# Performance work log

Hardware: AMD Instinct MI355X
Metric: run time of the kernel (lower is better)

The kernel has to match this reference:

```python
import jax, jax.numpy as jnp
import numpy as np

# Channel pairs (disjoint), matching init_kwargs
PAIRS = np.array([[2 * i, 2 * i + 1] for i in range(16)], dtype=np.int32)  # [P, 2]


def setup_inputs() -> dict:
    key = jax.random.key(0)
    kx, km = jax.random.split(key)
    B, C, T = 128, 64, 8000
    X = jax.random.normal(kx, (B, C, T), dtype=jnp.float32)
    # p_symmetry = 0.5 Bernoulli swap mask, precomputed (original uses numpy rng)
    swap_mask = jax.random.bernoulli(km, 0.5, (B, PAIRS.shape[0]))  # [B, P] bool
    return {"X": X, "swap_mask": swap_mask}


def reference(X, swap_mask):
    # X: [B, C, T], swap_mask: [B, P] bool
    B, C, T = X.shape
    c1 = jnp.asarray(PAIRS[:, 0])  # [P]
    c2 = jnp.asarray(PAIRS[:, 1])  # [P]
    # Build a per-batch channel permutation: identity, except swapped pairs.
    perm = jnp.broadcast_to(jnp.arange(C, dtype=jnp.int32), (B, C))
    perm = perm.at[:, c1].set(jnp.where(swap_mask, c2[None, :], c1[None, :]))
    perm = perm.at[:, c2].set(jnp.where(swap_mask, c1[None, :], c2[None, :]))
    # Single fused gather over the channel axis: [B, C, T]
    return jnp.take_along_axis(X, perm[:, :, None], axis=1)
```

## Files before the change

### kernel.cpp

```cpp
#include <hip/hip_runtime.h>


#define B_DIM 128
#define C_DIM 64
#define T_DIM 8000
#define T4    (T_DIM / 4)
#define P_DIM 16

typedef float f4 __attribute__((ext_vector_type(4)));

__global__ __launch_bounds__(256) void
ChannelSymmetry_42339787603992_kernel(const f4* __restrict__ X,
                                      const unsigned char* __restrict__ mask,
                                      f4* __restrict__ Y) {
    const int row = blockIdx.x;
    const int b   = row >> 6;
    const int c   = row & 63;

    __shared__ int s_bytepacked;
    if (threadIdx.x == 0) s_bytepacked = 0;
    __syncthreads();
    {
        const unsigned int w = ((const unsigned int*)mask)[threadIdx.x];
        const bool hit = (w & 0xFFFFFF00u) != 0;
        if (__any(hit) && (threadIdx.x & 63) == 0) atomicOr(&s_bytepacked, 1);
    }
    __syncthreads();

    int sc = c;
    if (c < 32) {
        const int ms = s_bytepacked ? 1 : 4;
        const unsigned char sw = mask[(b * P_DIM + (c >> 1)) * ms];
        if (sw) sc = c ^ 1;
    }

    const f4* __restrict__ src = X + (size_t)((b << 6) | sc) * T4;
    f4* __restrict__       dst = Y + (size_t)row * T4;
    for (int col = threadIdx.x; col < T4; col += 256) {
        const f4 v = __builtin_nontemporal_load(&src[col]);
        __builtin_nontemporal_store(v, &dst[col]);
    }
}

extern "C" void kernel_launch(void* const* d_in, const int* in_sizes, int n_in,
                              void* d_out, int out_size, void* d_ws, size_t ws_size,
                              hipStream_t stream) {
    const f4*            X    = (const f4*)d_in[0];
    const unsigned char* mask = (const unsigned char*)d_in[1];
    f4*                  Y    = (f4*)d_out;

    const int grid = B_DIM * C_DIM;
    ChannelSymmetry_42339787603992_kernel<<<grid, 256, 0, stream>>>(X, mask, Y);
}
```

Before: 98.30 us.

## Flatten gather to one float4 per thread across a global grid

Replaces the one-block-per-row loop with a flat grid in which each thread copies a single float4, working out row and column by division. The mask-layout detection now uses a wavefront vote instead of shared memory with atomics and two barriers, and the nontemporal load/store builtins are dropped in favour of plain accesses. The aim is to remove per-block barrier overhead and the tail imbalance of 2000 float4 spread over 256 threads, in exchange for many more blocks, a per-thread integer divide, and a redundant mask read in every thread.

```diff
diff --git a/kernel.cpp b/kernel.cpp
--- a/kernel.cpp
+++ b/kernel.cpp
@@ -6,6 +6,7 @@
 #define T_DIM 8000
 #define T4    (T_DIM / 4)
 #define P_DIM 16
+#define N_F4  (B_DIM * C_DIM * T4)
 
 typedef float f4 __attribute__((ext_vector_type(4)));
 
@@ -13,33 +14,23 @@
 ChannelSymmetry_42339787603992_kernel(const f4* __restrict__ X,
                                       const unsigned char* __restrict__ mask,
                                       f4* __restrict__ Y) {
-    const int row = blockIdx.x;
-    const int b   = row >> 6;
-    const int c   = row & 63;
+    const unsigned g = blockIdx.x * 256u + threadIdx.x;
 
-    __shared__ int s_bytepacked;
-    if (threadIdx.x == 0) s_bytepacked = 0;
-    __syncthreads();
-    {
-        const unsigned int w = ((const unsigned int*)mask)[threadIdx.x];
-        const bool hit = (w & 0xFFFFFF00u) != 0;
-        if (__any(hit) && (threadIdx.x & 63) == 0) atomicOr(&s_bytepacked, 1);
-    }
-    __syncthreads();
+    const unsigned lane_word = ((const unsigned*)mask)[threadIdx.x & 63];
+    const bool bytepacked = __any((lane_word & 0xFFFFFF00u) != 0);
 
-    int sc = c;
-    if (c < 32) {
-        const int ms = s_bytepacked ? 1 : 4;
-        const unsigned char sw = mask[(b * P_DIM + (c >> 1)) * ms];
-        if (sw) sc = c ^ 1;
+    const unsigned row = g / 2000u;
+    const unsigned col = g - row * 2000u;
+    const unsigned b   = row >> 6;
+    const unsigned c   = row & 63u;
+
+    unsigned sc = c;
+    if (c < 32u) {
+        const unsigned off = (b * P_DIM + (c >> 1)) << (bytepacked ? 0 : 2);
+        if (mask[off]) sc = c ^ 1u;
     }
 
-    const f4* __restrict__ src = X + (size_t)((b << 6) | sc) * T4;
-    f4* __restrict__       dst = Y + (size_t)row * T4;
-    for (int col = threadIdx.x; col < T4; col += 256) {
-        const f4 v = __builtin_nontemporal_load(&src[col]);
-        __builtin_nontemporal_store(v, &dst[col]);
-    }
+    Y[(size_t)row * T4 + col] = X[(size_t)((b << 6) | sc) * T4 + col];
 }
 
 extern "C" void kernel_launch(void* const* d_in, const int* in_sizes, int n_in,
@@ -49,6 +40,6 @@
     const unsigned char* mask = (const unsigned char*)d_in[1];
     f4*                  Y    = (f4*)d_out;
 
-    const int grid = B_DIM * C_DIM;
+    const int grid = N_F4 / 256;
     ChannelSymmetry_42339787603992_kernel<<<grid, 256, 0, stream>>>(X, mask, Y);
 }
```

After: 92.32 us. 1.06x faster.
